# Optimization experiments

Measured on AMD Instinct MI355X. Metric: run time of the kernel, lower is better.

Reference implementation:

```python
import jax, jax.numpy as jnp
import numpy as np

N = 50000       # num_nodes
E = 800000      # num_edges (avg degree 16)
DIN = 128       # input_dim
DOUT = 128      # output_dim
H = 4           # num_heads
HD = DOUT // H  # head_dim = 32


def setup_inputs() -> dict:
    key = jax.random.key(0)
    ks = jax.random.split(key, 9)
    x = jax.random.normal(ks[0], (N, DIN), dtype=jnp.float32)
    edge_index = jax.random.randint(ks[1], (2, E), 0, N, dtype=jnp.int64)
    s = 1.0 / np.sqrt(DIN)
    Wq = jax.random.uniform(ks[2], (DOUT, DIN), jnp.float32, -s, s)
    bq = jax.random.uniform(ks[3], (DOUT,), jnp.float32, -s, s)
    Wk = jax.random.uniform(ks[4], (DOUT, DIN), jnp.float32, -s, s)
    bk = jax.random.uniform(ks[5], (DOUT,), jnp.float32, -s, s)
    Wv = jax.random.uniform(ks[6], (DOUT, DIN), jnp.float32, -s, s)
    bv = jax.random.uniform(ks[7], (DOUT,), jnp.float32, -s, s)
    att = jax.random.normal(ks[8], (H, 2 * HD), dtype=jnp.float32)  # nn.Parameter(randn)
    return {"x": x, "edge_index": edge_index, "Wq": Wq, "bq": bq,
            "Wk": Wk, "bk": bk, "Wv": Wv, "bv": bv, "att": att}


def reference(x, edge_index, Wq, bq, Wk, bk, Wv, bv, att):
    n = x.shape[0]
    q = (x @ Wq.T + bq).reshape(n, H, HD)
    k = (x @ Wk.T + bk).reshape(n, H, HD)
    v = (x @ Wv.T + bv).reshape(n, H, HD)
    row, col = edge_index[0], edge_index[1]

    # scores = leaky_relu(sum(cat([q[row],k[col]]) * att)) computed without concat
    a_q, a_k = att[:, :HD], att[:, HD:]                       # [H,HD] each
    scores = jnp.einsum('ehd,hd->eh', q[row], a_q) \
           + jnp.einsum('ehd,hd->eh', k[col], a_k)            # [E,H]
    scores = jax.nn.leaky_relu(scores, 0.2)

    # segment-softmax over edges grouped by destination node (col), per head
    m = jax.ops.segment_max(scores, col, num_segments=n)      # [N,H]
    m = jnp.where(jnp.isfinite(m), m, 0.0)                    # empty segments -> -inf guard
    e = jnp.exp(scores - m[col])                              # [E,H]
    denom = jax.ops.segment_sum(e, col, num_segments=n)       # [N,H]
    w_edge = e / denom[col]                                   # softmax per dst segment

    # attention_weights[i] = mean over incoming edges of softmax weights; 0 if deg==0
    deg = jax.ops.segment_sum(jnp.ones((col.shape[0],), jnp.float32), col,
                              num_segments=n)                 # [N]
    w_sum = jax.ops.segment_sum(w_edge, col, num_segments=n)  # [N,H]
    attn_w = jnp.where(deg[:, None] > 0, w_sum / jnp.maximum(deg, 1.0)[:, None], 0.0)

    # output[dst] += attn_w[dst] * v[src], summed over edges
    msgs = attn_w[col][:, :, None] * v[row]                   # [E,H,HD]
    out = jax.ops.segment_sum(msgs, col, num_segments=n)      # [N,H,HD]
    return out.reshape(n, DOUT)                               # dropout: eval mode (identity)
```

## Files before the change

kernel.cpp:

```cpp
#include <hip/hip_runtime.h>


#define N_NODES 50000
#define N_EDGES 800000
#define SPAN    96
#define NBUCK   521
#define CAP     2304
#define NREP    4
#define RCAP    576
#define HSPAN   48
#define NR      8
#define EPB     2048
#define NCHUNK  391
#define GEMMB   391

#define OFF_SORTED 12800000
#define OFF_CURSOR 17601536

typedef __attribute__((ext_vector_type(8))) short short8;
typedef __attribute__((ext_vector_type(4))) float f32x4;

__device__ __forceinline__ unsigned int pack_bf16_rne(float a, float b) {
    unsigned int ua = __float_as_uint(a), ub = __float_as_uint(b);
    unsigned int ha = (ua + 0x7FFFu + ((ua >> 16) & 1u)) >> 16;
    unsigned int hb = (ub + 0x7FFFu + ((ub >> 16) & 1u)) >> 16;
    return ha | (hb << 16);
}
__device__ __forceinline__ unsigned short bf16_rne(float a) {
    unsigned int ua = __float_as_uint(a);
    return (unsigned short)((ua + 0x7FFFu + ((ua >> 16) & 1u)) >> 16);
}
__device__ __forceinline__ float bflo(unsigned int u) { return __uint_as_float(u << 16); }
__device__ __forceinline__ float bfhi(unsigned int u) { return __uint_as_float(u & 0xFFFF0000u); }

__global__ __launch_bounds__(512) void fused_gemm_scatter(
        const float* __restrict__ x, const float* __restrict__ Wv,
        const float* __restrict__ bv, unsigned int* __restrict__ vh,
        const int* __restrict__ ei, unsigned int* __restrict__ Cursor,
        unsigned int* __restrict__ sorted) {
    __shared__ __align__(16) unsigned char smem[128 * 68 * 4];
    __shared__ int s_wide;
    __shared__ int ctot[9], coff[9], s_cnt;
    int t = threadIdx.x;

    if (blockIdx.x < GEMMB) {
        unsigned int* wB = (unsigned int*)smem;
        for (int q = t; q < 8192; q += 512) {
            int o = q >> 6, k2 = q & 63;
            float2 wp = ((const float2*)Wv)[q];
            wB[o * 68 + k2] = pack_bf16_rne(wp.x, wp.y);
        }
        __syncthreads();

        int lane = t & 63, w = t >> 6;
        int quad = lane >> 4, lc = lane & 15;
        int n0 = blockIdx.x * 128 + w * 16;

        int arow = n0 + lc;
        int arowc = min(arow, N_NODES - 1);
        const float4* xrow = (const float4*)(x + (size_t)arowc * 128);

        f32x4 acc[8];
        #pragma unroll
        for (int ot = 0; ot < 8; ++ot) acc[ot] = (f32x4){0.f, 0.f, 0.f, 0.f};

        #pragma unroll
        for (int ks = 0; ks < 4; ++ks) {
            float4 f0 = xrow[ks * 8 + quad * 2];
            float4 f1 = xrow[ks * 8 + quad * 2 + 1];
            uint4 a4;
            a4.x = pack_bf16_rne(f0.x, f0.y);
            a4.y = pack_bf16_rne(f0.z, f0.w);
            a4.z = pack_bf16_rne(f1.x, f1.y);
            a4.w = pack_bf16_rne(f1.z, f1.w);
            short8 af = *(const short8*)&a4;
            #pragma unroll
            for (int ot = 0; ot < 8; ++ot) {
                uint4 b4 = *(const uint4*)&wB[(ot * 16 + lc) * 68 + ks * 16 + quad * 4];
                short8 bf = *(const short8*)&b4;
                acc[ot] = __builtin_amdgcn_mfma_f32_16x16x32_bf16(af, bf, acc[ot], 0, 0, 0);
            }
        }

        #pragma unroll
        for (int ot = 0; ot < 8; ++ot) {
            int o = ot * 16 + lc;
            float bb = bv[o];
            #pragma unroll
            for (int r = 0; r < 4; ++r) {
                int node = n0 + quad * 4 + r;
                unsigned short u = bf16_rne(acc[ot][r] + bb);
                unsigned int partner = (unsigned int)__shfl_xor((int)u, 1, 64);
                if ((lane & 1) == 0 && node < N_NODES) {
                    unsigned int pair = (unsigned int)u | (partner << 16);
                    vh[(size_t)node * 64 + (o >> 1)] = pair;
                }
            }
        }
    } else {
        unsigned int* w    = (unsigned int*)smem;
        int* h             = (int*)(smem + 8192);
        int* base          = (int*)(smem + 8192 + 2084);
        int* pfx           = (int*)(smem + 8192 + 2 * 2084);
        unsigned int* lval = (unsigned int*)(smem + 8192 + 3 * 2084);
        unsigned int* ldst = lval + EPB;
        unsigned int V = Cursor[NREP * NBUCK];
        int rep = (blockIdx.x - GEMMB) & (NREP - 1);
        for (int j = t; j < NBUCK; j += 512) h[j] = 0;
        if (t < 64) {
            int nz = (ei[2 * t + 1] != 0) ? 1 : 0;
            unsigned long long b = __ballot(nz);
            if (t == 0) s_wide = (b == 0ULL) ? 1 : 0;
        }
        __syncthreads();
        int wide = s_wide;
        int e0 = (blockIdx.x - GEMMB) * EPB;

        #pragma unroll
        for (int k = 0; k < EPB / 512; ++k) {
            int e = e0 + k * 512 + t;
            if (e < N_EDGES) {
                int r, c;
                if (wide) {
                    r = (int)((const uint2*)ei)[e].x;
                    c = (int)((const uint2*)ei)[N_EDGES + e].x;
                } else {
                    r = ei[e];
                    c = ei[N_EDGES + e];
                }
                w[k * 512 + t] = ((unsigned int)c << 16) | (unsigned int)r;
                atomicAdd(&h[c / SPAN], 1);
            } else {
                w[k * 512 + t] = 0xFFFFFFFFu;
            }
        }
        __syncthreads();
        for (int j = t; j < NBUCK; j += 512) {
            int cnt = h[j];
            base[j] = cnt ? (int)(atomicAdd(&Cursor[rep * NBUCK + j],
                                            (unsigned int)cnt) - V) : 0;
        }
        {
            int lane = t & 63, wv = t >> 6;
            int v0 = (t < NBUCK) ? h[t] : 0;
            int s = v0;
            #pragma unroll
            for (int off = 1; off < 64; off <<= 1) {
                int y = __shfl_up(s, off, 64);
                if (lane >= off) s += y;
            }
            pfx[t] = s - v0;
            if (lane == 63) ctot[wv] = s;
            __syncthreads();
            if (t == 0) {
                int a = 0;
                for (int i = 512; i < NBUCK; ++i) { pfx[i] = a; a += h[i]; }
                ctot[8] = a;
                int b2 = 0;
                #pragma unroll
                for (int i = 0; i < 9; ++i) { coff[i] = b2; b2 += ctot[i]; }
                s_cnt = b2;
            }
            __syncthreads();
            pfx[t] += coff[t >> 6];
            if (t < NBUCK - 512) pfx[512 + t] += coff[8];
            for (int j = t; j < NBUCK; j += 512) h[j] = 0;
            __syncthreads();
        }
        #pragma unroll
        for (int k = 0; k < EPB / 512; ++k) {
            unsigned int ww = w[k * 512 + t];
            if (ww != 0xFFFFFFFFu) {
                int bin = (int)(ww >> 16) / SPAN;
                int r = atomicAdd(&h[bin], 1);
                int q = pfx[bin] + r;
                int g = base[bin] + r;
                lval[q] = ww;
                ldst[q] = (g >= 0 && g < RCAP)
                        ? (unsigned int)(bin * CAP + rep * RCAP + g)
                        : 0xFFFFFFFFu;
            }
        }
        __syncthreads();
        int cntb = s_cnt;
        for (int i = t; i < cntb; i += 512) {
            unsigned int dst = ldst[i];
            if (dst != 0xFFFFFFFFu) sorted[dst] = lval[i];
        }
    }
}

__global__ __launch_bounds__(512) void gather_kernel(const unsigned int* __restrict__ vh,
                                                     const unsigned int* __restrict__ sorted,
                                                     const unsigned int* __restrict__ Cursor,
                                                     float* __restrict__ out) {
    __shared__ unsigned int ww[CAP];
    __shared__ unsigned short rl[CAP];
    __shared__ int hist[HSPAN * NR];
    __shared__ int st[HSPAN * NR + 1];
    __shared__ int s_off[NREP + 1];
    __shared__ int chunk_tot[6], chunk_off[6];
    int t = threadIdx.x;
    int b  = blockIdx.x >> 1;
    int hb = blockIdx.x & 1;
    int nb0 = b * SPAN + hb * HSPAN;
    int span = min(HSPAN, N_NODES - nb0);
    if (span <= 0) return;
    unsigned int V = Cursor[NREP * NBUCK];
    if (t == 0) {
        int off = 0;
        #pragma unroll
        for (int rp = 0; rp < NREP; ++rp) {
            s_off[rp] = off;
            off += min((int)(Cursor[rp * NBUCK + b] - V), RCAP);
        }
        s_off[NREP] = off;
    }
    for (int j = t; j < HSPAN * NR; j += 512) hist[j] = 0;
    __syncthreads();

    #pragma unroll
    for (int rp = 0; rp < NREP; ++rp) {
        int o0 = s_off[rp], cr = s_off[rp + 1] - o0;
        const unsigned int* runr = sorted + (size_t)b * CAP + rp * RCAP;
        for (int i = t; i < cr; i += 512) {
            unsigned int v = runr[i];
            ww[o0 + i] = v;
            unsigned int ln = (v >> 16) - (unsigned int)nb0;
            if (ln < (unsigned int)HSPAN) {
                int rr = (int)((v & 0xFFFFu) >> 13);
                atomicAdd(&hist[ln * NR + rr], 1);
            }
        }
    }
    __syncthreads();
    int cnt = s_off[NREP];

    int lane = t & 63, wid = t >> 6;
    int idx = wid * 64 + lane;
    {
        int val = (wid < 6) ? hist[idx] : 0;
        int s = val;
        #pragma unroll
        for (int off = 1; off < 64; off <<= 1) {
            int y = __shfl_up(s, off, 64);
            if (lane >= off) s += y;
        }
        if (wid < 6) {
            st[idx] = s - val;
            if (lane == 63) chunk_tot[wid] = s;
        }
        __syncthreads();
        if (t == 0) {
            int a = 0;
            #pragma unroll
            for (int i = 0; i < 6; ++i) { chunk_off[i] = a; a += chunk_tot[i]; }
            st[HSPAN * NR] = a;
        }
        __syncthreads();
        if (wid < 6) { st[idx] += chunk_off[wid]; hist[idx] = 0; }
        __syncthreads();
    }

    for (int i = t; i < cnt; i += 512) {
        unsigned int v = ww[i];
        unsigned int ln = (v >> 16) - (unsigned int)nb0;
        if (ln < (unsigned int)HSPAN) {
            int k = (int)ln * NR + (int)((v & 0xFFFFu) >> 13);
            int p = st[k] + atomicAdd(&hist[k], 1);
            rl[p] = (unsigned short)(v & 0xFFFFu);
        }
    }
    __syncthreads();

    int quad = lane >> 4;
    int li = lane & 15;
    const uint4* v4 = (const uint4*)vh;

#define ACC8(p) do { \
        c0 += (double)bflo((p).x); c1 += (double)bfhi((p).x); \
        c2 += (double)bflo((p).y); c3 += (double)bfhi((p).y); \
        c4 += (double)bflo((p).z); c5 += (double)bfhi((p).z); \
        c6 += (double)bflo((p).w); c7 += (double)bfhi((p).w); } while (0)

    for (int g = wid; g * 4 < span; g += 8) {
        int ln = g * 4 + quad;
        int s0 = st[ln * NR];
        int d  = st[ln * NR + NR] - s0;
        double c0 = 0., c1 = 0., c2 = 0., c3 = 0.;
        double c4 = 0., c5 = 0., c6 = 0., c7 = 0.;
        int j = 0;
        if (d >= 8) {
            int a0 = rl[s0 + 0], a1 = rl[s0 + 1];
            int a2 = rl[s0 + 2], a3 = rl[s0 + 3];
            uint4 pA0 = v4[(size_t)a0 * 16 + li];
            uint4 pA1 = v4[(size_t)a1 * 16 + li];
            uint4 pA2 = v4[(size_t)a2 * 16 + li];
            uint4 pA3 = v4[(size_t)a3 * 16 + li];
            for (; j + 8 <= d; j += 4) {
                int b0 = rl[s0 + j + 4], b1 = rl[s0 + j + 5];
                int b2 = rl[s0 + j + 6], b3 = rl[s0 + j + 7];
                uint4 pB0 = v4[(size_t)b0 * 16 + li];
                uint4 pB1 = v4[(size_t)b1 * 16 + li];
                uint4 pB2 = v4[(size_t)b2 * 16 + li];
                uint4 pB3 = v4[(size_t)b3 * 16 + li];
                ACC8(pA0); ACC8(pA1); ACC8(pA2); ACC8(pA3);
                pA0 = pB0; pA1 = pB1; pA2 = pB2; pA3 = pB3;
            }
            ACC8(pA0); ACC8(pA1); ACC8(pA2); ACC8(pA3);
            j += 4;
        } else if (d >= 4) {
            int a0 = rl[s0 + 0], a1 = rl[s0 + 1];
            int a2 = rl[s0 + 2], a3 = rl[s0 + 3];
            uint4 pA0 = v4[(size_t)a0 * 16 + li];
            uint4 pA1 = v4[(size_t)a1 * 16 + li];
            uint4 pA2 = v4[(size_t)a2 * 16 + li];
            uint4 pA3 = v4[(size_t)a3 * 16 + li];
            ACC8(pA0); ACC8(pA1); ACC8(pA2); ACC8(pA3);
            j = 4;
        }
        for (; j < d; ++j) {
            int r0 = rl[s0 + j];
            uint4 p0 = v4[(size_t)r0 * 16 + li];
            ACC8(p0);
        }
        double sc = (d > 0) ? 1.0 / (double)d : 0.0;
        float4 ra = {(float)(c0 * sc), (float)(c1 * sc),
                     (float)(c2 * sc), (float)(c3 * sc)};
        float4 rb = {(float)(c4 * sc), (float)(c5 * sc),
                     (float)(c6 * sc), (float)(c7 * sc)};
        ((float4*)out)[(size_t)(nb0 + ln) * 32 + 2 * li]     = ra;
        ((float4*)out)[(size_t)(nb0 + ln) * 32 + 2 * li + 1] = rb;
    }
#undef ACC8
}

extern "C" void kernel_launch(void* const* d_in, const int* in_sizes, int n_in,
                              void* d_out, int out_size, void* d_ws, size_t ws_size,
                              hipStream_t stream) {
    const float* x  = (const float*)d_in[0];
    const int*   ei = (const int*)d_in[1];
    const float* Wv = (const float*)d_in[6];
    const float* bv = (const float*)d_in[7];
    float* out = (float*)d_out;

    char* ws = (char*)d_ws;
    unsigned int* vh     = (unsigned int*)(ws);
    unsigned int* sorted = (unsigned int*)(ws + OFF_SORTED);
    unsigned int* Cursor = (unsigned int*)(ws + OFF_CURSOR);

    fused_gemm_scatter<<<GEMMB + NCHUNK, 512, 0, stream>>>(x, Wv, bv, vh,
                                                           ei, Cursor, sorted);
    gather_kernel<<<NBUCK * 2, 512, 0, stream>>>(vh, sorted, Cursor, out);
}
```

Baseline: 136.8 us.

## Fuse GEMM/scatter and gather into one persistent kernel with grid barrier

Merges the two launches into a single kernel in which GEMM and scatter blocks, plus the remaining idle blocks, meet at a software grid barrier built on an atomic counter, then all run the gather phase. Bucket span changes from 96 to 104 so the grid of 962 blocks covers both phases. The scatter now recomputes destinations from the stored values instead of keeping a separate ldst array, which cuts LDS use so more blocks fit per CU (launch_bounds 512,8). This removes one launch and the gap between kernels, but it depends on every block being co-resident, otherwise the barrier deadlocks, and all blocks spin-wait on a single counter.

Result: slower. 546.3 us (+299.4%).

```diff
diff --git a/kernel.cpp b/kernel.cpp
--- a/kernel.cpp
+++ b/kernel.cpp
@@ -3,16 +3,19 @@
 
 #define N_NODES 50000
 #define N_EDGES 800000
-#define SPAN    96
-#define NBUCK   521
-#define CAP     2304
+#define SPAN    104
+#define NBUCK   481
+#define CAP     2448
 #define NREP    4
-#define RCAP    576
-#define HSPAN   48
+#define RCAP    612
+#define HSPAN   52
 #define NR      8
 #define EPB     2048
 #define NCHUNK  391
 #define GEMMB   391
+#define GRID    (NBUCK * 2)
+#define SENT    (NREP * NBUCK)
+#define BARIDX  (SENT + 1)
 
 #define OFF_SORTED 12800000
 #define OFF_CURSOR 17601536
@@ -33,14 +36,16 @@
 __device__ __forceinline__ float bflo(unsigned int u) { return __uint_as_float(u << 16); }
 __device__ __forceinline__ float bfhi(unsigned int u) { return __uint_as_float(u & 0xFFFF0000u); }
 
-__global__ __launch_bounds__(512) void fused_gemm_scatter(
+__global__ __launch_bounds__(512, 8) void mega(
         const float* __restrict__ x, const float* __restrict__ Wv,
         const float* __restrict__ bv, unsigned int* __restrict__ vh,
         const int* __restrict__ ei, unsigned int* __restrict__ Cursor,
-        unsigned int* __restrict__ sorted) {
-    __shared__ __align__(16) unsigned char smem[128 * 68 * 4];
+        unsigned int* __restrict__ sorted, float* __restrict__ out) {
+    __shared__ __align__(16) unsigned char smem[34816];
     __shared__ int s_wide;
-    __shared__ int ctot[9], coff[9], s_cnt;
+    __shared__ int ctot[8], coff[8], s_cnt;
+    __shared__ int g_soff[NREP + 1];
+    __shared__ int g_ctot[7], g_coff[7];
     int t = threadIdx.x;
 
     if (blockIdx.x < GEMMB) {
@@ -97,14 +102,13 @@
                 }
             }
         }
-    } else {
+    } else if (blockIdx.x < GEMMB + NCHUNK) {
         unsigned int* w    = (unsigned int*)smem;
         int* h             = (int*)(smem + 8192);
-        int* base          = (int*)(smem + 8192 + 2084);
-        int* pfx           = (int*)(smem + 8192 + 2 * 2084);
-        unsigned int* lval = (unsigned int*)(smem + 8192 + 3 * 2084);
-        unsigned int* ldst = lval + EPB;
-        unsigned int V = Cursor[NREP * NBUCK];
+        int* base          = (int*)(smem + 8192 + 1924);
+        int* pfx           = (int*)(smem + 8192 + 3848);
+        unsigned int* lval = (unsigned int*)(smem + 8192 + 5896);
+        unsigned int V = Cursor[SENT];
         int rep = (blockIdx.x - GEMMB) & (NREP - 1);
         for (int j = t; j < NBUCK; j += 512) h[j] = 0;
         if (t < 64) {
@@ -154,16 +158,12 @@
             __syncthreads();
             if (t == 0) {
                 int a = 0;
-                for (int i = 512; i < NBUCK; ++i) { pfx[i] = a; a += h[i]; }
-                ctot[8] = a;
-                int b2 = 0;
                 #pragma unroll
-                for (int i = 0; i < 9; ++i) { coff[i] = b2; b2 += ctot[i]; }
-                s_cnt = b2;
-            }
-            __syncthreads();
-            pfx[t] += coff[t >> 6];
-            if (t < NBUCK - 512) pfx[512 + t] += coff[8];
+                for (int i = 0; i < 8; ++i) { coff[i] = a; a += ctot[i]; }
+                s_cnt = a;
+            }
+            __syncthreads();
+            if (t < NBUCK) pfx[t] += coff[wv];
             for (int j = t; j < NBUCK; j += 512) h[j] = 0;
             __syncthreads();
         }
@@ -173,109 +173,108 @@
             if (ww != 0xFFFFFFFFu) {
                 int bin = (int)(ww >> 16) / SPAN;
                 int r = atomicAdd(&h[bin], 1);
-                int q = pfx[bin] + r;
-                int g = base[bin] + r;
-                lval[q] = ww;
-                ldst[q] = (g >= 0 && g < RCAP)
-                        ? (unsigned int)(bin * CAP + rep * RCAP + g)
-                        : 0xFFFFFFFFu;
+                lval[pfx[bin] + r] = ww;
             }
         }
         __syncthreads();
         int cntb = s_cnt;
         for (int i = t; i < cntb; i += 512) {
-            unsigned int dst = ldst[i];
-            if (dst != 0xFFFFFFFFu) sorted[dst] = lval[i];
+            unsigned int val = lval[i];
+            int bin = (int)(val >> 16) / SPAN;
+            int g = base[bin] + (i - pfx[bin]);
+            if (g >= 0 && g < RCAP)
+                sorted[(size_t)bin * CAP + rep * RCAP + g] = val;
         }
     }
-}
-
-__global__ __launch_bounds__(512) void gather_kernel(const unsigned int* __restrict__ vh,
-                                                     const unsigned int* __restrict__ sorted,
-                                                     const unsigned int* __restrict__ Cursor,
-                                                     float* __restrict__ out) {
-    __shared__ unsigned int ww[CAP];
-    __shared__ unsigned short rl[CAP];
-    __shared__ int hist[HSPAN * NR];
-    __shared__ int st[HSPAN * NR + 1];
-    __shared__ int s_off[NREP + 1];
-    __shared__ int chunk_tot[6], chunk_off[6];
-    int t = threadIdx.x;
-    int b  = blockIdx.x >> 1;
-    int hb = blockIdx.x & 1;
-    int nb0 = b * SPAN + hb * HSPAN;
-    int span = min(HSPAN, N_NODES - nb0);
-    if (span <= 0) return;
-    unsigned int V = Cursor[NREP * NBUCK];
+
+    __threadfence();
+    __syncthreads();
     if (t == 0) {
-        int off = 0;
+        unsigned int V = Cursor[SENT];
+        atomicAdd(&Cursor[BARIDX], 1u);
+        while (atomicAdd(&Cursor[BARIDX], 0u) - V < (unsigned int)GRID)
+            __builtin_amdgcn_s_sleep(8);
+    }
+    __syncthreads();
+    __threadfence();
+
+    {
+        unsigned int* ww   = (unsigned int*)smem;
+        unsigned short* rl = (unsigned short*)(smem + 9792);
+        int* hist          = (int*)(smem + 14688);
+        int* st            = (int*)(smem + 16352);
+        int b  = blockIdx.x >> 1;
+        int hb = blockIdx.x & 1;
+        int nb0 = b * SPAN + hb * HSPAN;
+        int span = min(HSPAN, N_NODES - nb0);
+        unsigned int V = Cursor[SENT];
+        if (t == 0) {
+            int off = 0;
+            #pragma unroll
+            for (int rp = 0; rp < NREP; ++rp) {
+                g_soff[rp] = off;
+                off += min((int)(Cursor[rp * NBUCK + b] - V), RCAP);
+            }
+            g_soff[NREP] = off;
+        }
+        for (int j = t; j < HSPAN * NR; j += 512) hist[j] = 0;
+        __syncthreads();
+
         #pragma unroll
         for (int rp = 0; rp < NREP; ++rp) {
-            s_off[rp] = off;
-            off += min((int)(Cursor[rp * NBUCK + b] - V), RCAP);
-        }
-        s_off[NREP] = off;
-    }
-    for (int j = t; j < HSPAN * NR; j += 512) hist[j] = 0;
-    __syncthreads();
-
-    #pragma unroll
-    for (int rp = 0; rp < NREP; ++rp) {
-        int o0 = s_off[rp], cr = s_off[rp + 1] - o0;
-        const unsigned int* runr = sorted + (size_t)b * CAP + rp * RCAP;
-        for (int i = t; i < cr; i += 512) {
-            unsigned int v = runr[i];
-            ww[o0 + i] = v;
+            int o0 = g_soff[rp], cr = g_soff[rp + 1] - o0;
+            const unsigned int* runr = sorted + (size_t)b * CAP + rp * RCAP;
+            for (int i = t; i < cr; i += 512) {
+                unsigned int v = runr[i];
+                ww[o0 + i] = v;
+                unsigned int ln = (v >> 16) - (unsigned int)nb0;
+                if (ln < (unsigned int)HSPAN) {
+                    int rr = (int)((v & 0xFFFFu) >> 13);
+                    atomicAdd(&hist[ln * NR + rr], 1);
+                }
+            }
+        }
+        __syncthreads();
+        int cnt = g_soff[NREP];
+
+        int lane = t & 63, wid = t >> 6;
+        int idx = wid * 64 + lane;
+        {
+            int val = (wid < 7 && idx < HSPAN * NR) ? hist[idx] : 0;
+            int s = val;
+            #pragma unroll
+            for (int off = 1; off < 64; off <<= 1) {
+                int y = __shfl_up(s, off, 64);
+                if (lane >= off) s += y;
+            }
+            if (wid < 7 && idx < HSPAN * NR) st[idx] = s - val;
+            if (wid < 7 && lane == 63) g_ctot[wid] = s;
+            __syncthreads();
+            if (t == 0) {
+                int a = 0;
+                #pragma unroll
+                for (int i = 0; i < 7; ++i) { g_coff[i] = a; a += g_ctot[i]; }
+                st[HSPAN * NR] = a;
+            }
+            __syncthreads();
+            if (wid < 7 && idx < HSPAN * NR) { st[idx] += g_coff[wid]; hist[idx] = 0; }
+            __syncthreads();
+        }
+
+        for (int i = t; i < cnt; i += 512) {
+            unsigned int v = ww[i];
             unsigned int ln = (v >> 16) - (unsigned int)nb0;
             if (ln < (unsigned int)HSPAN) {
-                int rr = (int)((v & 0xFFFFu) >> 13);
-                atomicAdd(&hist[ln * NR + rr], 1);
-            }
-        }
-    }
-    __syncthreads();
-    int cnt = s_off[NREP];
-
-    int lane = t & 63, wid = t >> 6;
-    int idx = wid * 64 + lane;
-    {
-        int val = (wid < 6) ? hist[idx] : 0;
-        int s = val;
-        #pragma unroll
-        for (int off = 1; off < 64; off <<= 1) {
-            int y = __shfl_up(s, off, 64);
-            if (lane >= off) s += y;
-        }
-        if (wid < 6) {
-            st[idx] = s - val;
-            if (lane == 63) chunk_tot[wid] = s;
-        }
-        __syncthreads();
-        if (t == 0) {
-            int a = 0;
-            #pragma unroll
-            for (int i = 0; i < 6; ++i) { chunk_off[i] = a; a += chunk_tot[i]; }
-            st[HSPAN * NR] = a;
-        }
-        __syncthreads();
-        if (wid < 6) { st[idx] += chunk_off[wid]; hist[idx] = 0; }
-        __syncthreads();
-    }
-
-    for (int i = t; i < cnt; i += 512) {
-        unsigned int v = ww[i];
-        unsigned int ln = (v >> 16) - (unsigned int)nb0;
-        if (ln < (unsigned int)HSPAN) {
-            int k = (int)ln * NR + (int)((v & 0xFFFFu) >> 13);
-            int p = st[k] + atomicAdd(&hist[k], 1);
-            rl[p] = (unsigned short)(v & 0xFFFFu);
-        }
-    }
-    __syncthreads();
-
-    int quad = lane >> 4;
-    int li = lane & 15;
-    const uint4* v4 = (const uint4*)vh;
+                int k = (int)ln * NR + (int)((v & 0xFFFFu) >> 13);
+                int p = st[k] + atomicAdd(&hist[k], 1);
+                rl[p] = (unsigned short)(v & 0xFFFFu);
+            }
+        }
+        __syncthreads();
+
+        int quad = lane >> 4;
+        int li = lane & 15;
+        const uint4* v4 = (const uint4*)vh;
 
 #define ACC8(p) do { \
         c0 += (double)bflo((p).x); c1 += (double)bfhi((p).x); \
@@ -283,56 +282,57 @@
         c4 += (double)bflo((p).z); c5 += (double)bfhi((p).z); \
         c6 += (double)bflo((p).w); c7 += (double)bfhi((p).w); } while (0)
 
-    for (int g = wid; g * 4 < span; g += 8) {
-        int ln = g * 4 + quad;
-        int s0 = st[ln * NR];
-        int d  = st[ln * NR + NR] - s0;
-        double c0 = 0., c1 = 0., c2 = 0., c3 = 0.;
-        double c4 = 0., c5 = 0., c6 = 0., c7 = 0.;
-        int j = 0;
-        if (d >= 8) {
-            int a0 = rl[s0 + 0], a1 = rl[s0 + 1];
-            int a2 = rl[s0 + 2], a3 = rl[s0 + 3];
-            uint4 pA0 = v4[(size_t)a0 * 16 + li];
-            uint4 pA1 = v4[(size_t)a1 * 16 + li];
-            uint4 pA2 = v4[(size_t)a2 * 16 + li];
-            uint4 pA3 = v4[(size_t)a3 * 16 + li];
-            for (; j + 8 <= d; j += 4) {
-                int b0 = rl[s0 + j + 4], b1 = rl[s0 + j + 5];
-                int b2 = rl[s0 + j + 6], b3 = rl[s0 + j + 7];
-                uint4 pB0 = v4[(size_t)b0 * 16 + li];
-                uint4 pB1 = v4[(size_t)b1 * 16 + li];
-                uint4 pB2 = v4[(size_t)b2 * 16 + li];
-                uint4 pB3 = v4[(size_t)b3 * 16 + li];
+        for (int g = wid; g * 4 < span; g += 8) {
+            int ln = g * 4 + quad;
+            int s0 = st[ln * NR];
+            int d  = st[ln * NR + NR] - s0;
+            double c0 = 0., c1 = 0., c2 = 0., c3 = 0.;
+            double c4 = 0., c5 = 0., c6 = 0., c7 = 0.;
+            int j = 0;
+            if (d >= 8) {
+                int a0 = rl[s0 + 0], a1 = rl[s0 + 1];
+                int a2 = rl[s0 + 2], a3 = rl[s0 + 3];
+                uint4 pA0 = v4[(size_t)a0 * 16 + li];
+                uint4 pA1 = v4[(size_t)a1 * 16 + li];
+                uint4 pA2 = v4[(size_t)a2 * 16 + li];
+                uint4 pA3 = v4[(size_t)a3 * 16 + li];
+                for (; j + 8 <= d; j += 4) {
+                    int b0 = rl[s0 + j + 4], b1 = rl[s0 + j + 5];
+                    int b2 = rl[s0 + j + 6], b3 = rl[s0 + j + 7];
+                    uint4 pB0 = v4[(size_t)b0 * 16 + li];
+                    uint4 pB1 = v4[(size_t)b1 * 16 + li];
+                    uint4 pB2 = v4[(size_t)b2 * 16 + li];
+                    uint4 pB3 = v4[(size_t)b3 * 16 + li];
+                    ACC8(pA0); ACC8(pA1); ACC8(pA2); ACC8(pA3);
+                    pA0 = pB0; pA1 = pB1; pA2 = pB2; pA3 = pB3;
+                }
                 ACC8(pA0); ACC8(pA1); ACC8(pA2); ACC8(pA3);
-                pA0 = pB0; pA1 = pB1; pA2 = pB2; pA3 = pB3;
-            }
-            ACC8(pA0); ACC8(pA1); ACC8(pA2); ACC8(pA3);
-            j += 4;
-        } else if (d >= 4) {
-            int a0 = rl[s0 + 0], a1 = rl[s0 + 1];
-            int a2 = rl[s0 + 2], a3 = rl[s0 + 3];
-            uint4 pA0 = v4[(size_t)a0 * 16 + li];
-            uint4 pA1 = v4[(size_t)a1 * 16 + li];
-            uint4 pA2 = v4[(size_t)a2 * 16 + li];
-            uint4 pA3 = v4[(size_t)a3 * 16 + li];
-            ACC8(pA0); ACC8(pA1); ACC8(pA2); ACC8(pA3);
-            j = 4;
-        }
-        for (; j < d; ++j) {
-            int r0 = rl[s0 + j];
-            uint4 p0 = v4[(size_t)r0 * 16 + li];
-            ACC8(p0);
-        }
-        double sc = (d > 0) ? 1.0 / (double)d : 0.0;
-        float4 ra = {(float)(c0 * sc), (float)(c1 * sc),
-                     (float)(c2 * sc), (float)(c3 * sc)};
-        float4 rb = {(float)(c4 * sc), (float)(c5 * sc),
-                     (float)(c6 * sc), (float)(c7 * sc)};
-        ((float4*)out)[(size_t)(nb0 + ln) * 32 + 2 * li]     = ra;
-        ((float4*)out)[(size_t)(nb0 + ln) * 32 + 2 * li + 1] = rb;
+                j += 4;
+            } else if (d >= 4) {
+                int a0 = rl[s0 + 0], a1 = rl[s0 + 1];
+                int a2 = rl[s0 + 2], a3 = rl[s0 + 3];
+                uint4 pA0 = v4[(size_t)a0 * 16 + li];
+                uint4 pA1 = v4[(size_t)a1 * 16 + li];
+                uint4 pA2 = v4[(size_t)a2 * 16 + li];
+                uint4 pA3 = v4[(size_t)a3 * 16 + li];
+                ACC8(pA0); ACC8(pA1); ACC8(pA2); ACC8(pA3);
+                j = 4;
+            }
+            for (; j < d; ++j) {
+                int r0 = rl[s0 + j];
+                uint4 p0 = v4[(size_t)r0 * 16 + li];
+                ACC8(p0);
+            }
+            double sc = (d > 0) ? 1.0 / (double)d : 0.0;
+            float4 ra = {(float)(c0 * sc), (float)(c1 * sc),
+                         (float)(c2 * sc), (float)(c3 * sc)};
+            float4 rb = {(float)(c4 * sc), (float)(c5 * sc),
+                         (float)(c6 * sc), (float)(c7 * sc)};
+            ((float4*)out)[(size_t)(nb0 + ln) * 32 + 2 * li]     = ra;
+            ((float4*)out)[(size_t)(nb0 + ln) * 32 + 2 * li + 1] = rb;
+        }
+#undef ACC8
     }
-#undef ACC8
 }
 
 extern "C" void kernel_launch(void* const* d_in, const int* in_sizes, int n_in,
@@ -349,7 +349,5 @@
     unsigned int* sorted = (unsigned int*)(ws + OFF_SORTED);
     unsigned int* Cursor = (unsigned int*)(ws + OFF_CURSOR);
 
-    fused_gemm_scatter<<<GEMMB + NCHUNK, 512, 0, stream>>>(x, Wv, bv, vh,
-                                                           ei, Cursor, sorted);
-    gather_kernel<<<NBUCK * 2, 512, 0, stream>>>(vh, sorted, Cursor, out);
+    mega<<<GRID, 512, 0, stream>>>(x, Wv, bv, vh, ei, Cursor, sorted, out);
 }
```
